# Kernel tuning notes

Measured on AMD Instinct MI355X. Metric: run time of the kernel, lower is better.

## Reference

```python
import jax, jax.numpy as jnp
import numpy as np

T, N = 128, 32
C, HW = 4, 64
FEAT = 64 * 4 * 4  # 1024, conv output flattened
FC = 512
H = 256
A = 18


def _conv(x, w, b, stride):
    y = jax.lax.conv_general_dilated(x, w, (stride, stride), 'VALID',
                                     dimension_numbers=('NCHW', 'OIHW', 'NCHW'))
    return y + b[None, :, None, None]


def setup_inputs() -> dict:
    key = jax.random.key(0)
    ks = jax.random.split(key, 16)
    s = 0.05
    x = jax.random.uniform(ks[0], (T * N, C, HW, HW), jnp.float32, 0.0, 255.0)
    done = (jax.random.uniform(ks[1], (T * N,)) < 0.05).astype(jnp.float32)
    return {
        'x': x,
        'done': done,
        'h0': jnp.zeros((1, N, H), jnp.float32),
        'c0': jnp.zeros((1, N, H), jnp.float32),
        'conv1_w': jax.random.normal(ks[2], (32, C, 8, 8), jnp.float32) * s,
        'conv1_b': jnp.zeros((32,), jnp.float32),
        'conv2_w': jax.random.normal(ks[3], (64, 32, 4, 4), jnp.float32) * s,
        'conv2_b': jnp.zeros((64,), jnp.float32),
        'conv3_w': jax.random.normal(ks[4], (64, 64, 3, 3), jnp.float32) * s,
        'conv3_b': jnp.zeros((64,), jnp.float32),
        'fc_w': jax.random.normal(ks[5], (FC, FEAT), jnp.float32) * s,
        'fc_b': jnp.zeros((FC,), jnp.float32),
        'lstm_wi': jax.random.normal(ks[6], (4 * H, FC), jnp.float32) * s,
        'lstm_wh': jax.random.normal(ks[7], (4 * H, H), jnp.float32) * s,
        'lstm_bi': jnp.zeros((4 * H,), jnp.float32),
        'lstm_bh': jnp.zeros((4 * H,), jnp.float32),
        'actor_w': jax.random.normal(ks[8], (A, H), jnp.float32) * 0.01,
        'actor_b': jnp.zeros((A,), jnp.float32),
        'critic_w': jax.random.normal(ks[9], (1, H), jnp.float32) * s,
        'critic_b': jnp.zeros((1,), jnp.float32),
    }


def reference(x, done, h0, c0, conv1_w, conv1_b, conv2_w, conv2_b, conv3_w, conv3_b,
              fc_w, fc_b, lstm_wi, lstm_wh, lstm_bi, lstm_bh,
              actor_w, actor_b, critic_w, critic_b):
    # ---- CNN + FC encoder on all T*N frames at once ----
    z = x / 255.0
    z = jax.nn.relu(_conv(z, conv1_w, conv1_b, 4))   # (TN,32,15,15)
    z = jax.nn.relu(_conv(z, conv2_w, conv2_b, 2))   # (TN,64,6,6)
    z = jax.nn.relu(_conv(z, conv3_w, conv3_b, 1))   # (TN,64,4,4)
    z = z.reshape(z.shape[0], -1)                    # (TN,1024)
    feats = jax.nn.relu(z @ fc_w.T + fc_b)           # (TN,512)

    n_envs = h0.shape[1]
    feats = feats.reshape(-1, n_envs, feats.shape[-1])  # (T,N,512)
    dn = done.reshape(-1, n_envs)                        # (T,N)

    def step(carry, inp):
        h, c = carry
        f_t, d_t = inp
        m = (1.0 - d_t)[:, None]       # zero state at episode starts
        h = h * m
        c = c * m
        gates = f_t @ lstm_wi.T + lstm_bi + h @ lstm_wh.T + lstm_bh
        i, f, g, o = jnp.split(gates, 4, axis=-1)
        i, f, o = jax.nn.sigmoid(i), jax.nn.sigmoid(f), jax.nn.sigmoid(o)
        c = f * c + i * jnp.tanh(g)
        h = o * jnp.tanh(c)
        return (h, c), h

    (_, _), outs = jax.lax.scan(step, (h0[0], c0[0]), (feats, dn))  # outs (T,N,H)
    flat = outs.reshape(-1, outs.shape[-1])            # (TN,H)
    logits = flat @ actor_w.T + actor_b                # (TN,18)
    value = flat @ critic_w.T + critic_b               # (TN,1)
    return jnp.concatenate([logits, value], axis=-1)   # (TN,19)
```

## Files before the change

### kernel.cpp

```cpp
#include <hip/hip_runtime.h>
#include <math.h>


typedef _Float16 half2_t __attribute__((ext_vector_type(2)));

__device__ __forceinline__ float f4c(float4 v, int k) {
  return k == 0 ? v.x : (k == 1 ? v.y : (k == 2 ? v.z : v.w));
}

__global__ __launch_bounds__(256) void pack_w_kernel(
    const float* __restrict__ w1, const float* __restrict__ w2,
    float4* __restrict__ wp1, float4* __restrict__ wp2) {
  const int i = blockIdx.x * 256 + threadIdx.x;
  if (i < 2048) {
    const int og = i & 15, j = i >> 4;
    const int h = j & 3, jj = j >> 2;
    const int ky = jj & 7, c = jj >> 3;
    const float* b0 = w1 + (2 * og) * 256 + c * 64 + ky * 8 + 2 * h;
    const float* b1 = b0 + 256;
    wp1[i] = make_float4(b0[0], b1[0], b0[1], b1[1]);
  } else if (i < 10240) {
    const int i2 = i - 2048;
    const int op = i2 & 31, j = i2 >> 5;
    const int h = j & 1, jj = j >> 1;
    const int ky = jj & 3, c = jj >> 2;
    const float* b0 = w2 + (2 * op) * 512 + c * 16 + ky * 4 + 2 * h;
    const float* b1 = b0 + 512;
    wp2[i2] = make_float4(b0[0], b1[0], b0[1], b1[1]);
  }
}

__global__ __launch_bounds__(256) void conv1_kernel(
    const float* __restrict__ x, const float4* __restrict__ wp1,
    const float* __restrict__ bias, float* __restrict__ out) {
  __shared__ float xs[64 * 68];
  const int n = blockIdx.x;
  const int t = threadIdx.x;
  const int oy = t >> 4;
  const int og = t & 15;
  const int oc0 = og * 2;

  float acc[15][2] = {};
  const float4* xg = (const float4*)(x + (size_t)n * 16384);

  for (int c = 0; c < 4; ++c) {
    __syncthreads();
    #pragma unroll
    for (int i = 0; i < 4; ++i) {
      int f4 = i * 256 + t;
      int y = f4 >> 4, xq = f4 & 15;
      *(float4*)&xs[y * 68 + xq * 4] = xg[c * 1024 + f4];
    }
    __syncthreads();
    if (oy < 15) {
      for (int ky = 0; ky < 8; ++ky) {
        const float* xr = &xs[(4 * oy + ky) * 68];
        const float4* wb4 = wp1 + ((c * 8 + ky) * 4) * 16 + og;
        const float4 wv0 = wb4[0];
        const float4 wv1 = wb4[16];
        const float4 wv2 = wb4[32];
        const float4 wv3 = wb4[48];
        const float4 wv[4] = {wv0, wv1, wv2, wv3};
        {
          float4 xv[9];
          #pragma unroll
          for (int i = 0; i < 9; ++i) xv[i] = *(const float4*)(xr + 4 * i);
          #pragma unroll
          for (int h = 0; h < 4; ++h) {
            #pragma unroll
            for (int p = 0; p < 8; ++p) {
              const int k = 4 * p + 2 * h;
              const float xa = f4c(xv[k >> 2], k & 3);
              const float xb = f4c(xv[(k + 1) >> 2], (k + 1) & 3);
              acc[p][0] = fmaf(xa, wv[h].x, fmaf(xb, wv[h].z, acc[p][0]));
              acc[p][1] = fmaf(xa, wv[h].y, fmaf(xb, wv[h].w, acc[p][1]));
            }
          }
        }
        {
          float4 yv[8];
          #pragma unroll
          for (int i = 0; i < 8; ++i) yv[i] = *(const float4*)(xr + 32 + 4 * i);
          #pragma unroll
          for (int h = 0; h < 4; ++h) {
            #pragma unroll
            for (int p = 8; p < 15; ++p) {
              const int q = 4 * p + 2 * h - 32;
              const float xa = f4c(yv[q >> 2], q & 3);
              const float xb = f4c(yv[(q + 1) >> 2], (q + 1) & 3);
              acc[p][0] = fmaf(xa, wv[h].x, fmaf(xb, wv[h].z, acc[p][0]));
              acc[p][1] = fmaf(xa, wv[h].y, fmaf(xb, wv[h].w, acc[p][1]));
            }
          }
        }
      }
    }
  }
  if (oy < 15) {
    const float inv = 1.f / 255.f;
    #pragma unroll
    for (int o = 0; o < 2; ++o) {
      const int oc = oc0 + o;
      const float bb = bias[oc];
      float* orow = out + ((size_t)n * 32 + oc) * 225 + oy * 15;
      #pragma unroll
      for (int p = 0; p < 15; ++p)
        orow[p] = fmaxf(fmaf(acc[p][o], inv, bb), 0.f);
    }
  }
}

__global__ __launch_bounds__(192) void conv2_kernel(
    const float* __restrict__ a1, const float4* __restrict__ wp2,
    const float* __restrict__ bias, float* __restrict__ out) {
  __shared__ float xs[32 * 15 * 16];
  const int n = blockIdx.x;
  const int t = threadIdx.x;
  const float* ag = a1 + (size_t)n * 7200;
  for (int i = 0; i < 38; ++i) {
    int idx = i * 192 + t;
    if (idx < 7200) {
      int c = idx / 225, rem = idx - c * 225;
      int row = rem / 15, col = rem - row * 15;
      xs[(c * 15 + row) * 16 + col] = ag[idx];
    }
  }
  __syncthreads();

  const int oy = t >> 5;
  const int op = t & 31;
  const int oc0 = op * 2;
  float acc[6][2] = {};

  for (int c = 0; c < 32; ++c) {
    #pragma unroll
    for (int ky = 0; ky < 4; ++ky) {
      const float* xr = &xs[(c * 15 + 2 * oy + ky) * 16];
      const float4 xa = *(const float4*)(xr);
      const float4 xb = *(const float4*)(xr + 4);
      const float4 xc = *(const float4*)(xr + 8);
      const float2 xd = *(const float2*)(xr + 12);
      const float xv[14] = {xa.x, xa.y, xa.z, xa.w, xb.x, xb.y, xb.z, xb.w,
                            xc.x, xc.y, xc.z, xc.w, xd.x, xd.y};
      const float4 wA = wp2[((c * 4 + ky) * 2 + 0) * 32 + op];
      const float4 wB = wp2[((c * 4 + ky) * 2 + 1) * 32 + op];
      #pragma unroll
      for (int p = 0; p < 6; ++p) {
        const int b = 2 * p;
        acc[p][0] = fmaf(xv[b], wA.x, fmaf(xv[b + 1], wA.z,
                    fmaf(xv[b + 2], wB.x, fmaf(xv[b + 3], wB.z, acc[p][0]))));
        acc[p][1] = fmaf(xv[b], wA.y, fmaf(xv[b + 1], wA.w,
                    fmaf(xv[b + 2], wB.y, fmaf(xv[b + 3], wB.w, acc[p][1]))));
      }
    }
  }
  #pragma unroll
  for (int o = 0; o < 2; ++o) {
    const int oc = oc0 + o;
    const float bb = bias[oc];
    float* orow = out + ((size_t)n * 64 + oc) * 36 + oy * 6;
    #pragma unroll
    for (int p = 0; p < 6; ++p)
      orow[p] = fmaxf(acc[p][o] + bb, 0.f);
  }
}

__global__ __launch_bounds__(256) void conv3_kernel(
    const float* __restrict__ a2, const float* __restrict__ w,
    const float* __restrict__ bias, float* __restrict__ out) {
  __shared__ float wTs[144 * 65];
  __shared__ float xs2[64 * 36];
  const int n = blockIdx.x;
  const int t = threadIdx.x;
  const int oy = t >> 6;
  const int oc = t & 63;

  const float* ab = a2 + (size_t)n * 2304;
  #pragma unroll
  for (int i = 0; i < 9; ++i) xs2[i * 256 + t] = ab[i * 256 + t];

  float acc[4] = {};
  for (int c0 = 0; c0 < 64; c0 += 16) {
    __syncthreads();
    #pragma unroll
    for (int i = 0; i < 36; ++i) {
      const int lin = i * 256 + t;
      const int ocs = lin / 144;
      const int rem = lin - ocs * 144;
      wTs[rem * 65 + ocs] = w[(size_t)ocs * 576 + c0 * 9 + rem];
    }
    __syncthreads();
    for (int cc = 0; cc < 16; ++cc) {
      const float* xb = &xs2[(c0 + cc) * 36];
      #pragma unroll
      for (int ky = 0; ky < 3; ++ky) {
        const float* xr = xb + (oy + ky) * 6;
        const float2 x01 = *(const float2*)(xr);
        const float2 x23 = *(const float2*)(xr + 2);
        const float2 x45 = *(const float2*)(xr + 4);
        const float xv[6] = {x01.x, x01.y, x23.x, x23.y, x45.x, x45.y};
        const float* wrow = &wTs[(cc * 9 + ky * 3) * 65 + oc];
        const float wk0 = wrow[0], wk1 = wrow[65], wk2 = wrow[130];
        #pragma unroll
        for (int p = 0; p < 4; ++p)
          acc[p] = fmaf(xv[p], wk0,
                   fmaf(xv[p + 1], wk1,
                   fmaf(xv[p + 2], wk2, acc[p])));
      }
    }
  }
  const float bb = bias[oc];
  float* orow = out + ((size_t)n * 64 + oc) * 16 + oy * 4;
  #pragma unroll
  for (int p = 0; p < 4; ++p)
    orow[p] = fmaxf(acc[p] + bb, 0.f);
}

__global__ __launch_bounds__(256) void gemm_bias_kernel(
    const float* __restrict__ A, const float* __restrict__ B,
    const float* __restrict__ bias1, const float* __restrict__ bias2,
    float* __restrict__ C, int M, int N, int K, int relu) {
  __shared__ float As[16][68];
  __shared__ float Bs[16][68];
  const int t = threadIdx.x;
  const int n0 = blockIdx.x * 64;
  const int m0 = blockIdx.y * 64;
  const int ty = t >> 4, tx = t & 15;
  const int sl = t >> 2, kq = (t & 3) * 4;

  float acc[4][4] = {};

  for (int k0 = 0; k0 < K; k0 += 16) {
    float4 av = *(const float4*)(A + (size_t)(m0 + sl) * K + k0 + kq);
    float4 bv = *(const float4*)(B + (size_t)(n0 + sl) * K + k0 + kq);
    As[kq + 0][sl] = av.x; As[kq + 1][sl] = av.y;
    As[kq + 2][sl] = av.z; As[kq + 3][sl] = av.w;
    Bs[kq + 0][sl] = bv.x; Bs[kq + 1][sl] = bv.y;
    Bs[kq + 2][sl] = bv.z; Bs[kq + 3][sl] = bv.w;
    __syncthreads();
    #pragma unroll
    for (int kk = 0; kk < 16; ++kk) {
      float4 a = *(const float4*)&As[kk][ty * 4];
      float4 b = *(const float4*)&Bs[kk][tx * 4];
      float ar[4] = {a.x, a.y, a.z, a.w};
      float br[4] = {b.x, b.y, b.z, b.w};
      #pragma unroll
      for (int i = 0; i < 4; ++i)
        #pragma unroll
        for (int j = 0; j < 4; ++j)
          acc[i][j] = fmaf(ar[i], br[j], acc[i][j]);
    }
    __syncthreads();
  }

  #pragma unroll
  for (int i = 0; i < 4; ++i) {
    int m = m0 + ty * 4 + i;
    #pragma unroll
    for (int j = 0; j < 4; ++j) {
      int n = n0 + tx * 4 + j;
      float v = acc[i][j] + bias1[n];
      if (bias2) v += bias2[n];
      if (relu) v = fmaxf(v, 0.f);
      C[(size_t)m * N + n] = v;
    }
  }
}

__global__ __launch_bounds__(512, 2) void lstm_pair_kernel(
    const float* __restrict__ gates_pre, const float* __restrict__ wh,
    const float* __restrict__ done, const float* __restrict__ h0,
    const float* __restrict__ c0, float* __restrict__ outs,
    unsigned int* __restrict__ cnt, unsigned int* __restrict__ h2x) {
  __shared__ alignas(16) unsigned int h2s[128];
  __shared__ float pLDS[512];
  __shared__ float cLDS[128];
  __shared__ unsigned short hOut16[128];

  const int e = blockIdx.x & 31;
  const int s = blockIdx.x >> 5;
  const int rr = (int)threadIdx.x;
  const int g = rr >> 7;
  const int j = rr & 127;
  const int R = g * 256 + s * 128 + j;

  half2_t w2[128];
  {
    const float4* wr = (const float4*)(wh + (size_t)R * 256);
    #pragma unroll
    for (int i = 0; i < 64; ++i) {
      float4 f = wr[i];
      half2_t a, b;
      a.x = (_Float16)f.x; a.y = (_Float16)f.y;
      b.x = (_Float16)f.z; b.y = (_Float16)f.w;
      w2[2 * i] = a; w2[2 * i + 1] = b;
    }
  }

  if (rr < 128) {
    const float m0 = 1.f - done[e];
    float2 h = *(const float2*)(h0 + e * 256 + 2 * rr);
    half2_t hh; hh.x = (_Float16)(h.x * m0); hh.y = (_Float16)(h.y * m0);
    h2s[rr] = __builtin_bit_cast(unsigned int, hh);
    cLDS[rr] = c0[e * 256 + s * 128 + rr];
  }
  __syncthreads();

  const int my_off = s * 64;
  const int pa_off = 64 - my_off;

  for (int st = 0; st < 128; ++st) {
    const float gp = gates_pre[(size_t)(st * 32 + e) * 1024 + R];
    const float d_cur = done[st * 32 + e];
    const float d_nxt = (st < 127) ? done[(st + 1) * 32 + e] : 0.f;

    float a0 = 0.f, a1 = 0.f, a2 = 0.f, a3 = 0.f;
    #pragma unroll
    for (int i = 0; i < 8; ++i) {
      const uint4 hv0 = *(const uint4*)&h2s[4 * i];
      const uint4 hv1 = *(const uint4*)&h2s[32 + 4 * i];
      const uint4 hv2 = *(const uint4*)&h2s[64 + 4 * i];
      const uint4 hv3 = *(const uint4*)&h2s[96 + 4 * i];
      a0 = __builtin_amdgcn_fdot2(w2[4 * i + 0], __builtin_bit_cast(half2_t, hv0.x), a0, false);
      a1 = __builtin_amdgcn_fdot2(w2[32 + 4 * i + 0], __builtin_bit_cast(half2_t, hv1.x), a1, false);
      a2 = __builtin_amdgcn_fdot2(w2[64 + 4 * i + 0], __builtin_bit_cast(half2_t, hv2.x), a2, false);
      a3 = __builtin_amdgcn_fdot2(w2[96 + 4 * i + 0], __builtin_bit_cast(half2_t, hv3.x), a3, false);
      a0 = __builtin_amdgcn_fdot2(w2[4 * i + 1], __builtin_bit_cast(half2_t, hv0.y), a0, false);
      a1 = __builtin_amdgcn_fdot2(w2[32 + 4 * i + 1], __builtin_bit_cast(half2_t, hv1.y), a1, false);
      a2 = __builtin_amdgcn_fdot2(w2[64 + 4 * i + 1], __builtin_bit_cast(half2_t, hv2.y), a2, false);
      a3 = __builtin_amdgcn_fdot2(w2[96 + 4 * i + 1], __builtin_bit_cast(half2_t, hv3.y), a3, false);
      a0 = __builtin_amdgcn_fdot2(w2[4 * i + 2], __builtin_bit_cast(half2_t, hv0.z), a0, false);
      a1 = __builtin_amdgcn_fdot2(w2[32 + 4 * i + 2], __builtin_bit_cast(half2_t, hv1.z), a1, false);
      a2 = __builtin_amdgcn_fdot2(w2[64 + 4 * i + 2], __builtin_bit_cast(half2_t, hv2.z), a2, false);
      a3 = __builtin_amdgcn_fdot2(w2[96 + 4 * i + 2], __builtin_bit_cast(half2_t, hv3.z), a3, false);
      a0 = __builtin_amdgcn_fdot2(w2[4 * i + 3], __builtin_bit_cast(half2_t, hv0.w), a0, false);
      a1 = __builtin_amdgcn_fdot2(w2[32 + 4 * i + 3], __builtin_bit_cast(half2_t, hv1.w), a1, false);
      a2 = __builtin_amdgcn_fdot2(w2[64 + 4 * i + 3], __builtin_bit_cast(half2_t, hv2.w), a2, false);
      a3 = __builtin_amdgcn_fdot2(w2[96 + 4 * i + 3], __builtin_bit_cast(half2_t, hv3.w), a3, false);
    }
    pLDS[rr] = a0 + a1 + a2 + a3 + gp;
    __syncthreads();

    if (rr < 128) {
      const float m = 1.f - d_cur;
      float c = cLDS[rr] * m;
      float iv = pLDS[rr];
      float fv = pLDS[128 + rr];
      float gv = pLDS[256 + rr];
      float ov = pLDS[384 + rr];
      float ig = 1.f / (1.f + expf(-iv));
      float fg = 1.f / (1.f + expf(-fv));
      float og = 1.f / (1.f + expf(-ov));
      float cn = fmaf(fg, c, ig * tanhf(gv));
      float hn = og * tanhf(cn);
      cLDS[rr] = cn;
      outs[(size_t)st * 8192 + e * 256 + s * 128 + rr] = hn;
      hOut16[rr] = __builtin_bit_cast(unsigned short, (_Float16)hn);
    }
    __syncthreads();

    if (st < 127) {
      unsigned int* hx = h2x + (st & 1) * 4096 + e * 128;
      if (rr < 64) {
        unsigned int w = (unsigned int)hOut16[2 * rr] |
                         ((unsigned int)hOut16[2 * rr + 1] << 16);
        hx[my_off + rr] = w;
        h2s[my_off + rr] = (d_nxt != 0.f) ? 0u : w;
        __builtin_amdgcn_fence(__ATOMIC_RELEASE, "agent");
      }
      __syncthreads();
      if (rr == 0) {
        unsigned int* cp = &cnt[st * 32 + e];
        __hip_atomic_fetch_add(cp, 1u, __ATOMIC_RELAXED, __HIP_MEMORY_SCOPE_AGENT);
        while (__hip_atomic_load(cp, __ATOMIC_RELAXED, __HIP_MEMORY_SCOPE_AGENT) < 2u)
          __builtin_amdgcn_s_sleep(1);
      }
      __syncthreads();
      if (rr < 64) {
        __builtin_amdgcn_fence(__ATOMIC_ACQUIRE, "agent");
        unsigned int w = hx[pa_off + rr];
        h2s[pa_off + rr] = (d_nxt != 0.f) ? 0u : w;
      }
      __syncthreads();
    }
  }
}

__global__ __launch_bounds__(256) void heads_kernel(
    const float* __restrict__ outs, const float* __restrict__ aw,
    const float* __restrict__ ab, const float* __restrict__ cw,
    const float* __restrict__ cb, float* __restrict__ out) {
  __shared__ float rs[8 * 256];
  const int t = threadIdx.x;
  const int r0 = blockIdx.x * 8;
  for (int i = 0; i < 8; ++i)
    rs[i * 256 + t] = outs[(size_t)(r0 + i) * 256 + t];
  __syncthreads();
  int r = t >> 5, c = t & 31;
  if (c < 19) {
    const float* wr = (c < 18) ? (aw + c * 256) : cw;
    float bias = (c < 18) ? ab[c] : cb[0];
    float acc = 0.f;
    for (int k = 0; k < 256; ++k) acc = fmaf(rs[r * 256 + k], wr[k], acc);
    out[(size_t)(r0 + r) * 19 + c] = acc + bias;
  }
}

extern "C" void kernel_launch(void* const* d_in, const int* in_sizes, int n_in,
                              void* d_out, int out_size, void* d_ws, size_t ws_size,
                              hipStream_t stream) {
  (void)in_sizes; (void)n_in; (void)out_size;
  const float* x    = (const float*)d_in[0];
  const float* done = (const float*)d_in[1];
  const float* h0   = (const float*)d_in[2];
  const float* c0   = (const float*)d_in[3];
  const float* w1   = (const float*)d_in[4];
  const float* b1   = (const float*)d_in[5];
  const float* w2   = (const float*)d_in[6];
  const float* b2   = (const float*)d_in[7];
  const float* w3   = (const float*)d_in[8];
  const float* b3   = (const float*)d_in[9];
  const float* fcw  = (const float*)d_in[10];
  const float* fcb  = (const float*)d_in[11];
  const float* wi   = (const float*)d_in[12];
  const float* wh   = (const float*)d_in[13];
  const float* bi   = (const float*)d_in[14];
  const float* bh   = (const float*)d_in[15];
  const float* aw   = (const float*)d_in[16];
  const float* abv  = (const float*)d_in[17];
  const float* cw   = (const float*)d_in[18];
  const float* cbv  = (const float*)d_in[19];
  float* out = (float*)d_out;

  const size_t SZ_A1 = 29491200, SZ_A2 = 9437184, SZ_A3 = 4194304;
  const size_t SZ_F = 2097152, SZ_G = 4194304, SZ_O = 1048576;
  const size_t SZ_SYNC = 131072;
  const size_t need =
      (SZ_A1 + SZ_A2 + SZ_A3 + SZ_F + SZ_G + SZ_O + SZ_SYNC) * 4;
  if (ws_size < need) return;

  float* wsp  = (float*)d_ws;
  float* a1   = wsp;
  float* a2   = a1 + SZ_A1;
  float* a3   = a2 + SZ_A2;
  float* feats= a3 + SZ_A3;
  float* gts  = feats + SZ_F;
  float* outs = gts + SZ_G;
  float* syncb = outs + SZ_O;
  unsigned int* cnt = (unsigned int*)syncb;
  unsigned int* h2x = cnt + 4096;
  float4* wp1 = (float4*)(syncb + 16384);
  float4* wp2 = wp1 + 2048;

  (void)hipMemsetAsync(cnt, 0, 4096 * sizeof(unsigned int), stream);
  pack_w_kernel<<<40, 256, 0, stream>>>(w1, w2, wp1, wp2);
  conv1_kernel<<<4096, 256, 0, stream>>>(x, wp1, b1, a1);
  conv2_kernel<<<4096, 192, 0, stream>>>(a1, wp2, b2, a2);
  conv3_kernel<<<4096, 256, 0, stream>>>(a2, w3, b3, a3);
  gemm_bias_kernel<<<dim3(8, 64), 256, 0, stream>>>(a3, fcw, fcb, nullptr, feats,
                                                    4096, 512, 1024, 1);
  gemm_bias_kernel<<<dim3(16, 64), 256, 0, stream>>>(feats, wi, bi, bh, gts,
                                                     4096, 1024, 512, 0);
  lstm_pair_kernel<<<64, 512, 0, stream>>>(gts, wh, done, h0, c0, outs, cnt, h2x);
  heads_kernel<<<512, 256, 0, stream>>>(outs, aw, abv, cw, cbv, out);
}
```

Baseline: 1.444 ms.

## Run each env's LSTM in one 1024-thread block, dropping inter-block handshakes

Replaces the two-block-per-environment LSTM recurrence, which exchanged half of h through global memory with atomic counters and fences every step, with a single 1024-thread block per environment. Each thread holds one full gate row of W_h in fp16 registers, and 128 threads update two hidden units each, keeping c in registers and reading done flags from LDS. This removes the global exchange, the spin-wait and the memset, at the cost of using half as many CUs and needing 1024-thread occupancy with a 128-entry register weight array per thread.

```diff
diff --git a/kernel.cpp b/kernel.cpp
--- a/kernel.cpp
+++ b/kernel.cpp
@@ -267,26 +267,20 @@
   }
 }
 
-__global__ __launch_bounds__(512, 2) void lstm_pair_kernel(
+__global__ __launch_bounds__(1024, 1) void lstm_env_kernel(
     const float* __restrict__ gates_pre, const float* __restrict__ wh,
     const float* __restrict__ done, const float* __restrict__ h0,
-    const float* __restrict__ c0, float* __restrict__ outs,
-    unsigned int* __restrict__ cnt, unsigned int* __restrict__ h2x) {
+    const float* __restrict__ c0, float* __restrict__ outs) {
   __shared__ alignas(16) unsigned int h2s[128];
-  __shared__ float pLDS[512];
-  __shared__ float cLDS[128];
-  __shared__ unsigned short hOut16[128];
-
-  const int e = blockIdx.x & 31;
-  const int s = blockIdx.x >> 5;
-  const int rr = (int)threadIdx.x;
-  const int g = rr >> 7;
-  const int j = rr & 127;
-  const int R = g * 256 + s * 128 + j;
+  __shared__ float pLDS[1024];
+  __shared__ float dLDS[128];
+
+  const int e = blockIdx.x;
+  const int t = (int)threadIdx.x;
 
   half2_t w2[128];
   {
-    const float4* wr = (const float4*)(wh + (size_t)R * 256);
+    const float4* wr = (const float4*)(wh + (size_t)t * 256);
     #pragma unroll
     for (int i = 0; i < 64; ++i) {
       float4 f = wr[i];
@@ -297,22 +291,19 @@
     }
   }
 
-  if (rr < 128) {
+  float2 creg = make_float2(0.f, 0.f);
+  if (t < 128) {
+    dLDS[t] = done[t * 32 + e];
+    creg = *(const float2*)(c0 + e * 256 + 2 * t);
     const float m0 = 1.f - done[e];
-    float2 h = *(const float2*)(h0 + e * 256 + 2 * rr);
+    float2 h = *(const float2*)(h0 + e * 256 + 2 * t);
     half2_t hh; hh.x = (_Float16)(h.x * m0); hh.y = (_Float16)(h.y * m0);
-    h2s[rr] = __builtin_bit_cast(unsigned int, hh);
-    cLDS[rr] = c0[e * 256 + s * 128 + rr];
+    h2s[t] = __builtin_bit_cast(unsigned int, hh);
   }
   __syncthreads();
 
-  const int my_off = s * 64;
-  const int pa_off = 64 - my_off;
-
   for (int st = 0; st < 128; ++st) {
-    const float gp = gates_pre[(size_t)(st * 32 + e) * 1024 + R];
-    const float d_cur = done[st * 32 + e];
-    const float d_nxt = (st < 127) ? done[(st + 1) * 32 + e] : 0.f;
+    const float gp = gates_pre[(size_t)(st * 32 + e) * 1024 + t];
 
     float a0 = 0.f, a1 = 0.f, a2 = 0.f, a3 = 0.f;
     #pragma unroll
@@ -338,51 +329,35 @@
       a2 = __builtin_amdgcn_fdot2(w2[64 + 4 * i + 3], __builtin_bit_cast(half2_t, hv2.w), a2, false);
       a3 = __builtin_amdgcn_fdot2(w2[96 + 4 * i + 3], __builtin_bit_cast(half2_t, hv3.w), a3, false);
     }
-    pLDS[rr] = a0 + a1 + a2 + a3 + gp;
-    __syncthreads();
-
-    if (rr < 128) {
-      const float m = 1.f - d_cur;
-      float c = cLDS[rr] * m;
-      float iv = pLDS[rr];
-      float fv = pLDS[128 + rr];
-      float gv = pLDS[256 + rr];
-      float ov = pLDS[384 + rr];
-      float ig = 1.f / (1.f + expf(-iv));
-      float fg = 1.f / (1.f + expf(-fv));
-      float og = 1.f / (1.f + expf(-ov));
-      float cn = fmaf(fg, c, ig * tanhf(gv));
-      float hn = og * tanhf(cn);
-      cLDS[rr] = cn;
-      outs[(size_t)st * 8192 + e * 256 + s * 128 + rr] = hn;
-      hOut16[rr] = __builtin_bit_cast(unsigned short, (_Float16)hn);
-    }
-    __syncthreads();
-
-    if (st < 127) {
-      unsigned int* hx = h2x + (st & 1) * 4096 + e * 128;
-      if (rr < 64) {
-        unsigned int w = (unsigned int)hOut16[2 * rr] |
-                         ((unsigned int)hOut16[2 * rr + 1] << 16);
-        hx[my_off + rr] = w;
-        h2s[my_off + rr] = (d_nxt != 0.f) ? 0u : w;
-        __builtin_amdgcn_fence(__ATOMIC_RELEASE, "agent");
-      }
-      __syncthreads();
-      if (rr == 0) {
-        unsigned int* cp = &cnt[st * 32 + e];
-        __hip_atomic_fetch_add(cp, 1u, __ATOMIC_RELAXED, __HIP_MEMORY_SCOPE_AGENT);
-        while (__hip_atomic_load(cp, __ATOMIC_RELAXED, __HIP_MEMORY_SCOPE_AGENT) < 2u)
-          __builtin_amdgcn_s_sleep(1);
-      }
-      __syncthreads();
-      if (rr < 64) {
-        __builtin_amdgcn_fence(__ATOMIC_ACQUIRE, "agent");
-        unsigned int w = hx[pa_off + rr];
-        h2s[pa_off + rr] = (d_nxt != 0.f) ? 0u : w;
-      }
-      __syncthreads();
-    }
+    pLDS[t] = a0 + a1 + a2 + a3 + gp;
+    __syncthreads();
+
+    if (t < 128) {
+      const float m = 1.f - dLDS[st];
+      const float d_nxt = (st < 127) ? dLDS[st + 1] : 0.f;
+      const float c0r = creg.x * m, c1r = creg.y * m;
+      const float iv0 = pLDS[2 * t],       iv1 = pLDS[2 * t + 1];
+      const float fv0 = pLDS[256 + 2 * t], fv1 = pLDS[256 + 2 * t + 1];
+      const float gv0 = pLDS[512 + 2 * t], gv1 = pLDS[512 + 2 * t + 1];
+      const float ov0 = pLDS[768 + 2 * t], ov1 = pLDS[768 + 2 * t + 1];
+      const float ig0 = 1.f / (1.f + expf(-iv0));
+      const float ig1 = 1.f / (1.f + expf(-iv1));
+      const float fg0 = 1.f / (1.f + expf(-fv0));
+      const float fg1 = 1.f / (1.f + expf(-fv1));
+      const float og0 = 1.f / (1.f + expf(-ov0));
+      const float og1 = 1.f / (1.f + expf(-ov1));
+      const float cn0 = fmaf(fg0, c0r, ig0 * tanhf(gv0));
+      const float cn1 = fmaf(fg1, c1r, ig1 * tanhf(gv1));
+      const float hn0 = og0 * tanhf(cn0);
+      const float hn1 = og1 * tanhf(cn1);
+      creg.x = cn0; creg.y = cn1;
+      *(float2*)&outs[(size_t)st * 8192 + e * 256 + 2 * t] =
+          make_float2(hn0, hn1);
+      half2_t hh; hh.x = (_Float16)hn0; hh.y = (_Float16)hn1;
+      unsigned int w = __builtin_bit_cast(unsigned int, hh);
+      h2s[t] = (d_nxt != 0.f) ? 0u : w;
+    }
+    __syncthreads();
   }
 }
 
@@ -447,12 +422,9 @@
   float* gts  = feats + SZ_F;
   float* outs = gts + SZ_G;
   float* syncb = outs + SZ_O;
-  unsigned int* cnt = (unsigned int*)syncb;
-  unsigned int* h2x = cnt + 4096;
   float4* wp1 = (float4*)(syncb + 16384);
   float4* wp2 = wp1 + 2048;
 
-  (void)hipMemsetAsync(cnt, 0, 4096 * sizeof(unsigned int), stream);
   pack_w_kernel<<<40, 256, 0, stream>>>(w1, w2, wp1, wp2);
   conv1_kernel<<<4096, 256, 0, stream>>>(x, wp1, b1, a1);
   conv2_kernel<<<4096, 192, 0, stream>>>(a1, wp2, b2, a2);
@@ -461,6 +433,6 @@
                                                     4096, 512, 1024, 1);
   gemm_bias_kernel<<<dim3(16, 64), 256, 0, stream>>>(feats, wi, bi, bh, gts,
                                                      4096, 1024, 512, 0);
-  lstm_pair_kernel<<<64, 512, 0, stream>>>(gts, wh, done, h0, c0, outs, cnt, h2x);
+  lstm_env_kernel<<<32, 1024, 0, stream>>>(gts, wh, done, h0, c0, outs);
   heads_kernel<<<512, 256, 0, stream>>>(outs, aw, abv, cw, cbv, out);
 }
```

Measured after the change: 1.650 ms. 14.2% more time.
